# Kernel optimization log

Measured on AMD Instinct MI355X. Metric: run time of the kernel, lower is better.

Reference implementation:

```python
import jax, jax.numpy as jnp
import numpy as np

S, B, C = 7, 2, 20
LAMBDA_COORD, LAMBDA_NOOBJ = 5.0, 0.5
N, T = 16384, 32


def setup_inputs() -> dict:
    key = jax.random.key(0)
    k1, k2, k3 = jax.random.split(key, 3)
    outputs = jax.random.normal(k1, (N, S, S, B * 5 + C), dtype=jnp.float32)
    # center-format normalized boxes [x, y, w, h] in (0, 1)
    target_boxes = jax.random.uniform(k2, (N, T, 4), dtype=jnp.float32)
    target_labels = jax.random.randint(k3, (N, T), 0, C, dtype=jnp.int32)
    return {"outputs": outputs, "target_boxes": target_boxes, "target_labels": target_labels}


def _iou(b1, b2):
    # center-format boxes [..., 4] -> IoU, broadcasting over leading dims
    x11, y11 = b1[..., 0] - b1[..., 2] / 2, b1[..., 1] - b1[..., 3] / 2
    x12, y12 = b1[..., 0] + b1[..., 2] / 2, b1[..., 1] + b1[..., 3] / 2
    x21, y21 = b2[..., 0] - b2[..., 2] / 2, b2[..., 1] - b2[..., 3] / 2
    x22, y22 = b2[..., 0] + b2[..., 2] / 2, b2[..., 1] + b2[..., 3] / 2
    iw = jnp.clip(jnp.minimum(x12, x22) - jnp.maximum(x11, x21), 0.0)
    ih = jnp.clip(jnp.minimum(y12, y22) - jnp.maximum(y11, y21), 0.0)
    inter = iw * ih
    union = b1[..., 2] * b1[..., 3] + b2[..., 2] * b2[..., 3] - inter
    return inter / jnp.maximum(union, 1e-6)


def yolo_v1_loss(outputs, target_boxes, target_labels):
    n = outputs.shape[0]
    pred_boxes = outputs[..., : B * 4].reshape(n, S, S, B, 4)  # [n,S,S,B,4]
    pred_conf = outputs[..., B * 4 : B * 5]                    # [n,S,S,B]
    pred_cls = outputs[..., B * 5 :]                           # [n,S,S,C]

    cell = 1.0 / S
    g = jnp.arange(S, dtype=jnp.float32)
    px = (pred_boxes[..., 0] + g[None, None, :, None]) * cell  # grid_x varies along dim 2
    py = (pred_boxes[..., 1] + g[None, :, None, None]) * cell  # grid_y varies along dim 1
    pred_boxes_g = jnp.stack([px, py, pred_boxes[..., 2], pred_boxes[..., 3]], axis=-1)

    tx, ty, tw, th = (target_boxes[..., i] for i in range(4))
    gxi = jnp.clip((tx / cell).astype(jnp.int32), 0, S - 1)   # [n,T]
    gyi = jnp.clip((ty / cell).astype(jnp.int32), 0, S - 1)
    ox = (tx - gxi.astype(jnp.float32) * cell) / cell
    oy = (ty - gyi.astype(jnp.float32) * cell) / cell

    bidx = jnp.arange(n)[:, None]
    cell_boxes = pred_boxes_g[bidx, gyi, gxi]  # [n,T,B,4]
    cell_conf = pred_conf[bidx, gyi, gxi]      # [n,T,B]
    cell_cls = pred_cls[bidx, gyi, gxi]        # [n,T,C]

    ious = _iou(target_boxes[:, :, None, :], cell_boxes)          # [n,T,B]
    best = jnp.argmax(ious, axis=-1)                              # [n,T]
    best_box = jnp.take_along_axis(cell_boxes, best[..., None, None], axis=2)[:, :, 0]  # [n,T,4]
    best_conf = jnp.take_along_axis(cell_conf, best[..., None], axis=2)[:, :, 0]        # [n,T]

    pw = jnp.maximum(best_box[..., 2], 1e-6)
    ph = jnp.maximum(best_box[..., 3], 1e-6)
    twc = jnp.maximum(tw, 1e-6)
    thc = jnp.maximum(th, 1e-6)
    box_loss = (
        (best_box[..., 0] - ox) ** 2
        + (best_box[..., 1] - oy) ** 2
        + (jnp.sqrt(pw) - jnp.sqrt(twc)) ** 2
        + (jnp.sqrt(ph) - jnp.sqrt(thc)) ** 2
    ).sum(axis=1)                                                # per-image sum over targets

    obj_loss = ((best_conf - 1.0) ** 2).sum(axis=1)

    onehot = jax.nn.one_hot(target_labels, C, dtype=jnp.float32)
    class_loss = jnp.mean((jax.nn.softmax(cell_cls, axis=-1) - onehot) ** 2, axis=-1).sum(axis=1)

    # obj_mask is never set in the original, so noobj covers every cell/box
    noobj_loss = jnp.mean(pred_conf ** 2, axis=(1, 2, 3))

    per_img = LAMBDA_COORD * box_loss + class_loss + obj_loss + LAMBDA_NOOBJ * noobj_loss
    return jnp.mean(per_img)


def reference(outputs, target_boxes, target_labels):
    return yolo_v1_loss(outputs, target_boxes, target_labels)
```

## Files before the change

### kernel.cpp

```cpp
#include <hip/hip_runtime.h>
#include <math.h>

#define TPB 256
constexpr int kS = 7;
constexpr int kB = 2;
constexpr int kC = 20;
constexpr int kT = 32;
constexpr int kCH = kB * 5 + kC;
constexpr int kCells = kS * kS;
constexpr int kImgF = kCells * kCH;
constexpr int IMGS = 4;

__device__ __forceinline__ float block_reduce(float v, float* red) {
    #pragma unroll
    for (int off = 32; off > 0; off >>= 1)
        v += __shfl_down(v, off, 64);
    const int lane = threadIdx.x & 63;
    const int wave = threadIdx.x >> 6;
    if (lane == 0) red[wave] = v;
    __syncthreads();
    float s = 0.0f;
    if (threadIdx.x == 0) {
        #pragma unroll
        for (int w = 0; w < TPB / 64; w++) s += red[w];
    }
    return s;
}

__global__ __launch_bounds__(TPB) void yolo_stage1(
    const float* __restrict__ outputs,
    const float4* __restrict__ tboxes,
    const int* __restrict__ tlabels,
    float* __restrict__ blocksums,
    int n)
{
    __shared__ float red[TPB / 64];
    const int tid = threadIdx.x;
    const int img0 = blockIdx.x * IMGS;
    const int nimg = min(IMGS, n - img0);

    float local = 0.0f;
    const float kno = 0.5f / (float)(2 * kCells);

    const int pair = tid >> 1;
    const int b = tid & 1;
    const bool has_tgt = pair < nimg * kT;
    float4 tb = make_float4(0.f, 0.f, 0.f, 0.f);
    int lab = 0;
    if (has_tgt) {
        tb = tboxes[(size_t)img0 * kT + pair];
        lab = tlabels[(size_t)img0 * kT + pair];
    }

    if (nimg == IMGS) {
        const float4* src = reinterpret_cast<const float4*>(outputs + (size_t)img0 * kImgF);
        constexpr int NV4 = IMGS * kImgF / 4;
        constexpr int FULL = NV4 / TPB;
        float4 vv[FULL];
        #pragma unroll
        for (int i = 0; i < FULL; i++) vv[i] = src[tid + i * TPB];
        const int tidx = tid + FULL * TPB;
        float4 vt = make_float4(0.f, 0.f, 0.f, 0.f);
        const bool tok = tidx < NV4;
        if (tok) vt = src[tidx];

        int base = (4 * tid) % 30;
        #pragma unroll
        for (int i = 0; i < FULL; i++) {
            const float4 v = vv[i];
            if (base == 8)      local += kno * (v.x * v.x + v.y * v.y);
            else if (base == 6) local += kno * (v.z * v.z + v.w * v.w);
            base += 4; if (base >= 30) base -= 30;
        }
        if (tok) {
            if (base == 8)      local += kno * (vt.x * vt.x + vt.y * vt.y);
            else if (base == 6) local += kno * (vt.z * vt.z + vt.w * vt.w);
        }
    } else {
        const float* srcf = outputs + (size_t)img0 * kImgF;
        const int tot = nimg * kImgF;
        for (int i = tid; i < tot; i += TPB) {
            const float v = srcf[i];
            const int ch = i % kCH;
            if (ch == 8 || ch == 9) local += kno * v * v;
        }
    }

    if (has_tgt) {
        const int sub = pair >> 5;
        const float cellf = 1.0f / 7.0f;
        const float tx = tb.x, ty = tb.y, tw = tb.z, th = tb.w;

        int gxi = (int)(tx / cellf); gxi = min(max(gxi, 0), kS - 1);
        int gyi = (int)(ty / cellf); gyi = min(max(gyi, 0), kS - 1);
        const float ox = (tx - (float)gxi * cellf) / cellf;
        const float oy = (ty - (float)gyi * cellf) / cellf;
        const float2* __restrict__ cell2 = reinterpret_cast<const float2*>(
            outputs + (size_t)(img0 + sub) * kImgF + (gyi * kS + gxi) * kCH);

        const float2 xy = cell2[2 * b + 0];
        const float2 wh = cell2[2 * b + 1];
        const float2 cf = cell2[4];
        float cls[10];
        #pragma unroll
        for (int j = 0; j < 5; j++) {
            const float2 c2 = cell2[5 + 5 * b + j];
            cls[2 * j] = c2.x; cls[2 * j + 1] = c2.y;
        }

        const float t_x1 = tx - tw * 0.5f, t_x2 = tx + tw * 0.5f;
        const float t_y1 = ty - th * 0.5f, t_y2 = ty + th * 0.5f;
        const float px = (xy.x + (float)gxi) * cellf;
        const float py = (xy.y + (float)gyi) * cellf;
        const float x21 = px - wh.x * 0.5f, x22 = px + wh.x * 0.5f;
        const float y21 = py - wh.y * 0.5f, y22 = py + wh.y * 0.5f;
        const float iw = fmaxf(fminf(t_x2, x22) - fmaxf(t_x1, x21), 0.0f);
        const float ih = fmaxf(fminf(t_y2, y22) - fmaxf(t_y1, y21), 0.0f);
        const float inter = iw * ih;
        const float uni = tw * th + wh.x * wh.y - inter;
        const float iou_mine = inter / fmaxf(uni, 1e-6f);
        const float iou_other = __shfl_xor(iou_mine, 1, 64);
        const float iou0 = b ? iou_other : iou_mine;
        const float iou1 = b ? iou_mine : iou_other;
        const int best = (iou1 > iou0) ? 1 : 0;

        if (b == best) {
            const float pw = fmaxf(wh.x, 1e-6f), ph = fmaxf(wh.y, 1e-6f);
            const float twc = fmaxf(tw, 1e-6f), thc = fmaxf(th, 1e-6f);
            const float dx = px - ox, dy = py - oy;
            const float dws = sqrtf(pw) - sqrtf(twc), dhs = sqrtf(ph) - sqrtf(thc);
            const float box_loss = dx * dx + dy * dy + dws * dws + dhs * dhs;
            const float dconf = (b ? cf.y : cf.x) - 1.0f;
            local += 5.0f * box_loss + dconf * dconf;
        }

        float mh = cls[0];
        #pragma unroll
        for (int j = 1; j < 10; j++) mh = fmaxf(mh, cls[j]);
        const float m = fmaxf(mh, __shfl_xor(mh, 1, 64));
        float sh = 0.0f;
        #pragma unroll
        for (int j = 0; j < 10; j++) { cls[j] = __expf(cls[j] - m); sh += cls[j]; }
        const float ssum = sh + __shfl_xor(sh, 1, 64);
        const float inv = 1.0f / ssum;
        float cl = 0.0f;
        const int labh = lab - 10 * b;
        #pragma unroll
        for (int j = 0; j < 10; j++) {
            const float d = cls[j] * inv - (j == labh ? 1.0f : 0.0f);
            cl += d * d;
        }
        local += cl * (1.0f / (float)kC);
    }

    const float bsum = block_reduce(local, red);
    if (tid == 0) blocksums[blockIdx.x] = bsum;
}

__global__ __launch_bounds__(TPB) void yolo_stage2(
    const float* __restrict__ blocksums, int nblocks, float invn,
    float* __restrict__ out)
{
    __shared__ float red[TPB / 64];
    float local = 0.0f;
    for (int i = threadIdx.x; i < nblocks; i += TPB) local += blocksums[i];
    const float s = block_reduce(local, red);
    if (threadIdx.x == 0) out[0] = s * invn;
}

extern "C" void kernel_launch(void* const* d_in, const int* in_sizes, int n_in,
                              void* d_out, int out_size, void* d_ws, size_t ws_size,
                              hipStream_t stream)
{
    const float* outputs = (const float*)d_in[0];
    const float4* tboxes = (const float4*)d_in[1];
    const int* tlabels = (const int*)d_in[2];
    float* out = (float*)d_out;
    float* blocksums = (float*)d_ws;

    const int n = in_sizes[0] / kImgF;
    const int nblocks = (n + IMGS - 1) / IMGS;

    yolo_stage1<<<nblocks, TPB, 0, stream>>>(outputs, tboxes, tlabels, blocksums, n);
    yolo_stage2<<<1, TPB, 0, stream>>>(blocksums, nblocks, 1.0f / (float)n, out);
}
```

Measured before the change: 153.1 us.

## Fuse final reduction via last-block atomic counter and hoist target-cell gathers

Replaces the separate second-stage reduction kernel with a last-block-done pattern: each block stores its partial sum, increments an atomic counter, and the final block sums all partials. A memset resets the counter each launch. The gathered per-target cell loads are also moved up next to the bulk streaming loads so their latency overlaps. This trades one kernel launch for a memset node plus atomic and fence overhead.

```diff
diff --git a/kernel.cpp b/kernel.cpp
--- a/kernel.cpp
+++ b/kernel.cpp
@@ -27,14 +27,17 @@
     return s;
 }
 
-__global__ __launch_bounds__(TPB) void yolo_stage1(
+__global__ __launch_bounds__(TPB) void yolo_fused(
     const float* __restrict__ outputs,
     const float4* __restrict__ tboxes,
     const int* __restrict__ tlabels,
     float* __restrict__ blocksums,
-    int n)
+    unsigned int* __restrict__ counter,
+    float* __restrict__ out,
+    int n, float invn)
 {
     __shared__ float red[TPB / 64];
+    __shared__ int is_last;
     const int tid = threadIdx.x;
     const int img0 = blockIdx.x * IMGS;
     const int nimg = min(IMGS, n - img0);
@@ -52,18 +55,48 @@
         lab = tlabels[(size_t)img0 * kT + pair];
     }
 
-    if (nimg == IMGS) {
+    constexpr int NV4 = IMGS * kImgF / 4;
+    constexpr int FULL = NV4 / TPB;
+    float4 vv[FULL];
+    float4 vt = make_float4(0.f, 0.f, 0.f, 0.f);
+    bool tok = false;
+    const bool full_blk = (nimg == IMGS);
+    if (full_blk) {
         const float4* src = reinterpret_cast<const float4*>(outputs + (size_t)img0 * kImgF);
-        constexpr int NV4 = IMGS * kImgF / 4;
-        constexpr int FULL = NV4 / TPB;
-        float4 vv[FULL];
         #pragma unroll
         for (int i = 0; i < FULL; i++) vv[i] = src[tid + i * TPB];
         const int tidx = tid + FULL * TPB;
-        float4 vt = make_float4(0.f, 0.f, 0.f, 0.f);
-        const bool tok = tidx < NV4;
+        tok = tidx < NV4;
         if (tok) vt = src[tidx];
-
+    }
+
+    const float cellf = 1.0f / 7.0f;
+    int gxi = 0, gyi = 0;
+    float ox = 0.f, oy = 0.f;
+    float2 g_xy = make_float2(0.f, 0.f), g_wh = make_float2(0.f, 0.f);
+    float2 g_cf = make_float2(0.f, 0.f);
+    float cls[10];
+    #pragma unroll
+    for (int j = 0; j < 10; j++) cls[j] = 0.f;
+    if (has_tgt) {
+        const int sub = pair >> 5;
+        gxi = (int)(tb.x / cellf); gxi = min(max(gxi, 0), kS - 1);
+        gyi = (int)(tb.y / cellf); gyi = min(max(gyi, 0), kS - 1);
+        ox = (tb.x - (float)gxi * cellf) / cellf;
+        oy = (tb.y - (float)gyi * cellf) / cellf;
+        const float2* __restrict__ cell2 = reinterpret_cast<const float2*>(
+            outputs + (size_t)(img0 + sub) * kImgF + (gyi * kS + gxi) * kCH);
+        g_xy = cell2[2 * b + 0];
+        g_wh = cell2[2 * b + 1];
+        g_cf = cell2[4];
+        #pragma unroll
+        for (int j = 0; j < 5; j++) {
+            const float2 c2 = cell2[5 + 5 * b + j];
+            cls[2 * j] = c2.x; cls[2 * j + 1] = c2.y;
+        }
+    }
+
+    if (full_blk) {
         int base = (4 * tid) % 30;
         #pragma unroll
         for (int i = 0; i < FULL; i++) {
@@ -87,37 +120,18 @@
     }
 
     if (has_tgt) {
-        const int sub = pair >> 5;
-        const float cellf = 1.0f / 7.0f;
         const float tx = tb.x, ty = tb.y, tw = tb.z, th = tb.w;
-
-        int gxi = (int)(tx / cellf); gxi = min(max(gxi, 0), kS - 1);
-        int gyi = (int)(ty / cellf); gyi = min(max(gyi, 0), kS - 1);
-        const float ox = (tx - (float)gxi * cellf) / cellf;
-        const float oy = (ty - (float)gyi * cellf) / cellf;
-        const float2* __restrict__ cell2 = reinterpret_cast<const float2*>(
-            outputs + (size_t)(img0 + sub) * kImgF + (gyi * kS + gxi) * kCH);
-
-        const float2 xy = cell2[2 * b + 0];
-        const float2 wh = cell2[2 * b + 1];
-        const float2 cf = cell2[4];
-        float cls[10];
-        #pragma unroll
-        for (int j = 0; j < 5; j++) {
-            const float2 c2 = cell2[5 + 5 * b + j];
-            cls[2 * j] = c2.x; cls[2 * j + 1] = c2.y;
-        }
 
         const float t_x1 = tx - tw * 0.5f, t_x2 = tx + tw * 0.5f;
         const float t_y1 = ty - th * 0.5f, t_y2 = ty + th * 0.5f;
-        const float px = (xy.x + (float)gxi) * cellf;
-        const float py = (xy.y + (float)gyi) * cellf;
-        const float x21 = px - wh.x * 0.5f, x22 = px + wh.x * 0.5f;
-        const float y21 = py - wh.y * 0.5f, y22 = py + wh.y * 0.5f;
+        const float px = (g_xy.x + (float)gxi) * cellf;
+        const float py = (g_xy.y + (float)gyi) * cellf;
+        const float x21 = px - g_wh.x * 0.5f, x22 = px + g_wh.x * 0.5f;
+        const float y21 = py - g_wh.y * 0.5f, y22 = py + g_wh.y * 0.5f;
         const float iw = fmaxf(fminf(t_x2, x22) - fmaxf(t_x1, x21), 0.0f);
         const float ih = fmaxf(fminf(t_y2, y22) - fmaxf(t_y1, y21), 0.0f);
         const float inter = iw * ih;
-        const float uni = tw * th + wh.x * wh.y - inter;
+        const float uni = tw * th + g_wh.x * g_wh.y - inter;
         const float iou_mine = inter / fmaxf(uni, 1e-6f);
         const float iou_other = __shfl_xor(iou_mine, 1, 64);
         const float iou0 = b ? iou_other : iou_mine;
@@ -125,12 +139,12 @@
         const int best = (iou1 > iou0) ? 1 : 0;
 
         if (b == best) {
-            const float pw = fmaxf(wh.x, 1e-6f), ph = fmaxf(wh.y, 1e-6f);
+            const float pw = fmaxf(g_wh.x, 1e-6f), ph = fmaxf(g_wh.y, 1e-6f);
             const float twc = fmaxf(tw, 1e-6f), thc = fmaxf(th, 1e-6f);
             const float dx = px - ox, dy = py - oy;
             const float dws = sqrtf(pw) - sqrtf(twc), dhs = sqrtf(ph) - sqrtf(thc);
             const float box_loss = dx * dx + dy * dy + dws * dws + dhs * dhs;
-            const float dconf = (b ? cf.y : cf.x) - 1.0f;
+            const float dconf = (b ? g_cf.y : g_cf.x) - 1.0f;
             local += 5.0f * box_loss + dconf * dconf;
         }
 
@@ -154,18 +168,25 @@
     }
 
     const float bsum = block_reduce(local, red);
-    if (tid == 0) blocksums[blockIdx.x] = bsum;
-}
-
-__global__ __launch_bounds__(TPB) void yolo_stage2(
-    const float* __restrict__ blocksums, int nblocks, float invn,
-    float* __restrict__ out)
-{
-    __shared__ float red[TPB / 64];
-    float local = 0.0f;
-    for (int i = threadIdx.x; i < nblocks; i += TPB) local += blocksums[i];
-    const float s = block_reduce(local, red);
-    if (threadIdx.x == 0) out[0] = s * invn;
+
+    if (tid == 0) {
+        __hip_atomic_store(&blocksums[blockIdx.x], bsum,
+                           __ATOMIC_RELAXED, __HIP_MEMORY_SCOPE_AGENT);
+        __threadfence();
+        const unsigned int old = __hip_atomic_fetch_add(
+            counter, 1u, __ATOMIC_ACQ_REL, __HIP_MEMORY_SCOPE_AGENT);
+        is_last = (old == gridDim.x - 1) ? 1 : 0;
+    }
+    __syncthreads();
+    if (is_last) {
+        float l = 0.0f;
+        const int nb = gridDim.x;
+        for (int i = tid; i < nb; i += TPB)
+            l += __hip_atomic_load(&blocksums[i],
+                                   __ATOMIC_RELAXED, __HIP_MEMORY_SCOPE_AGENT);
+        const float s = block_reduce(l, red);
+        if (tid == 0) out[0] = s * invn;
+    }
 }
 
 extern "C" void kernel_launch(void* const* d_in, const int* in_sizes, int n_in,
@@ -181,6 +202,12 @@
     const int n = in_sizes[0] / kImgF;
     const int nblocks = (n + IMGS - 1) / IMGS;
 
-    yolo_stage1<<<nblocks, TPB, 0, stream>>>(outputs, tboxes, tlabels, blocksums, n);
-    yolo_stage2<<<1, TPB, 0, stream>>>(blocksums, nblocks, 1.0f / (float)n, out);
+    unsigned int* counter =
+        (unsigned int*)((char*)d_ws + (size_t)nblocks * sizeof(float));
+
+    hipMemsetAsync(counter, 0, sizeof(unsigned int), stream);
+
+    yolo_fused<<<nblocks, TPB, 0, stream>>>(outputs, tboxes, tlabels,
+                                            blocksums, counter, out,
+                                            n, 1.0f / (float)n);
 }
```

Result: slower. 478.0 us (+212.2%).
